# Performance work log

Hardware: AMD Instinct MI355X
Metric: run time of the kernel (lower is better)

Reference implementation:

```python
import jax, jax.numpy as jnp
import numpy as np

K = 3
HEADS = 6
EMBED = 192
KD = EMBED // HEADS  # 32
SCALE = float(KD) ** -0.5


def setup_inputs() -> dict:
    key = jax.random.key(0)
    ks = jax.random.split(key, 5)
    B, H, W, C = 8, 252, 192, 64
    x = jax.random.normal(ks[0], (B, H, W, C), dtype=jnp.float32)
    v_w = jax.random.normal(ks[1], (C, EMBED), dtype=jnp.float32) * (C ** -0.5)
    attn_w = jax.random.normal(ks[2], (C, K ** 4 * HEADS), dtype=jnp.float32) * (C ** -0.5)
    attn_b = jnp.zeros((K ** 4 * HEADS,), dtype=jnp.float32)
    out_w = jax.random.normal(ks[3], (EMBED, EMBED), dtype=jnp.float32) * (EMBED ** -0.5)
    out_b = jnp.zeros((EMBED,), dtype=jnp.float32)
    return {"x": x, "v_w": v_w, "attn_w": attn_w, "attn_b": attn_b,
            "out_w": out_w, "out_b": out_b}


def reference(x, v_w, attn_w, attn_b, out_w, out_b):
    B, H, W, C = x.shape
    hh, ww = -(-H // K), -(-W // K)          # ceil division
    ph, pw = hh * K - H, ww * K - W          # bottom/right zero padding
    xp = jnp.pad(x, ((0, 0), (0, ph), (0, pw), (0, 0))) if (ph or pw) else x

    # value branch: unfold into k*k windows -> [B, hh, ww, heads, k^2, kd]
    v = xp @ v_w
    v = v.reshape(B, hh, K, ww, K, HEADS, KD)
    v = v.transpose(0, 1, 3, 5, 2, 4, 6).reshape(B, hh, ww, HEADS, K * K, KD)

    # attention branch: k x k average pool (stride k) then dense to k^4*heads
    pooled = xp.reshape(B, hh, K, ww, K, C).mean(axis=(2, 4))  # [B, hh, ww, C]
    attn = (pooled @ attn_w + attn_b) * SCALE
    attn = attn.reshape(B, hh, ww, HEADS, K * K, K * K)
    attn = jax.nn.softmax(attn, axis=-1)

    # windowed attention: [.., k^2, k^2] @ [.., k^2, kd]
    out = attn @ v                                             # [B, hh, ww, heads, k^2, kd]

    # fold back to spatial layout, drop padding
    out = out.reshape(B, hh, ww, HEADS, K, K, KD)
    out = out.transpose(0, 1, 4, 2, 5, 3, 6).reshape(B, hh * K, ww * K, EMBED)
    out = out[:, :H, :W, :]
    return out @ out_w + out_b
```

## Files before the change

kernel.cpp:

```cpp
#include <hip/hip_runtime.h>
#include <hip/hip_bf16.h>

#define NB   8
#define NH   252
#define NW   192
#define NC   64
#define HHD  84
#define WWD  64
#define NE   192
#define NO   486
#define NWIN (NB*HHD*WWD)
#define SCALE_F 0.17677669529663687f

typedef __bf16 bf16x8 __attribute__((ext_vector_type(8)));
typedef __bf16 bf16x4 __attribute__((ext_vector_type(4)));
typedef float floatx4 __attribute__((ext_vector_type(4)));

__device__ __attribute__((aligned(16))) __hip_bfloat16 g_WT[NE * 384];
__device__ __attribute__((aligned(16))) __hip_bfloat16 g_awT[NO * 64];

__device__ __forceinline__ bf16x8 bf16x8_zero() {
    bf16x8 z;
    #pragma unroll
    for (int j = 0; j < 8; ++j) z[j] = (__bf16)0.f;
    return z;
}

__device__ __forceinline__ int koff(int t) {
    int v = 16 * t - 8;
    v = v < 0 ? 0 : v;
    return v > 48 ? 48 : v;
}

__global__ __launch_bounds__(256) void kt_prep(
    const float* __restrict__ vw, const float* __restrict__ ow,
    const float* __restrict__ aw)
{
    int t = blockIdx.x * 256 + threadIdx.x;
    if (t < NE * 384) {
        int e  = t / 384;
        int hc = t - e * 384;
        int h  = hc >> 6;
        int c  = hc & 63;
        float s = 0.f;
        #pragma unroll
        for (int d = 0; d < 32; ++d)
            s = fmaf(vw[c * NE + h * 32 + d], ow[(h * 32 + d) * NE + e], s);
        g_WT[e * 384 + hc] = __float2bfloat16(s);
    } else {
        int tt = t - NE * 384;
        if (tt < NO * 64) {
            int n = tt >> 6;
            int c = tt & 63;
            g_awT[tt] = __float2bfloat16(aw[c * NO + n]);
        }
    }
}

__global__ __launch_bounds__(256, 3) void ka_fused(
    const float* __restrict__ x,
    const float* __restrict__ attn_b,
    const float* __restrict__ out_b,
    float* __restrict__ out)
{
    __shared__ __attribute__((aligned(16))) __bf16 xwT[64 * 88];
    __shared__ __attribute__((aligned(16))) __bf16 attnA[6 * 5 * 16 * 32];
    __shared__ __attribute__((aligned(16))) __bf16 Ph[80 * 72];

    __bf16* pooledB = Ph;

    const int tid  = threadIdx.x;
    const int lane = tid & 63;
    const int wv   = tid >> 6;
    const int m16  = lane & 15;
    const int quad = lane >> 4;
    const int wbase = blockIdx.x * 8;

    const int bB   = wbase / 5376;
    const int remB = wbase - bB * 5376;
    const int iB   = remB >> 6;
    const int jB   = remB & 63;
    const int xbase = ((bB * NH + iB * 3) * NW + jB * 3) * NC;

    #pragma unroll
    for (int i = 0; i < 5; ++i) {
        int b4 = i * 4 + wv;
        bf16x4 pk;
        #pragma unroll
        for (int s = 0; s < 4; ++s) {
            int p10 = b4 * 4 + s;
            int w = p10 / 10;
            int q = p10 - w * 10;
            float xv = 0.f;
            if (q < 9) {
                int pr = q / 3;
                int pc = q - pr * 3;
                xv = x[xbase + (pr * NW + w * 3 + pc) * NC + lane];
            }
            pk[s] = (__bf16)xv;
        }
        *(bf16x4*)(&xwT[lane * 88 + b4 * 4]) = pk;
    }
    #pragma unroll
    for (int i = 0; i < 8; ++i) {
        int ch = i * 256 + tid;
        if (ch < 1920) *(uint4*)(&attnA[ch * 8]) = make_uint4(0u, 0u, 0u, 0u);
    }
    __syncthreads();

    #pragma unroll
    for (int i = 0; i < 2; ++i) {
        int win = i * 4 + wv;
        float s = 0.f;
        #pragma unroll
        for (int q = 0; q < 9; ++q) s += (float)xwT[lane * 88 + win * 10 + q];
        pooledB[win * 64 + lane] = (__bf16)(s * (1.f / 9.f));
    }
    __syncthreads();

    {
        bf16x8 afragP[2];
        #pragma unroll
        for (int ks = 0; ks < 2; ++ks)
            afragP[ks] = *(const bf16x8*)(&pooledB[m16 * 64 + ks * 32 + quad * 8]);
        const __bf16* Aw = (const __bf16*)g_awT;
        #pragma unroll
        for (int i = 0; i < 8; ++i) {
            int tile = wv * 8 + i;
            int n = tile * 16 + m16;
            bool nvalid = (tile < 31) && (n < NO);
            bf16x8 b0 = nvalid ? *(const bf16x8*)(Aw + n * 64 + quad * 8)      : bf16x8_zero();
            bf16x8 b1 = nvalid ? *(const bf16x8*)(Aw + n * 64 + 32 + quad * 8) : bf16x8_zero();
            floatx4 acc;
            acc[0] = 0.f; acc[1] = 0.f; acc[2] = 0.f; acc[3] = 0.f;
            acc = __builtin_amdgcn_mfma_f32_16x16x32_bf16(afragP[0], b0, acc, 0, 0, 0);
            acc = __builtin_amdgcn_mfma_f32_16x16x32_bf16(afragP[1], b1, acc, 0, 0, 0);
            if (nvalid && quad < 2) {
                float bn = attn_b[n];
                int h   = n / 81;
                int r81 = n - h * 81;
                int p   = r81 / 9;
                int q   = r81 - p * 9;
                #pragma unroll
                for (int r = 0; r < 4; ++r) {
                    int win = quad * 4 + r;
                    int R   = win * 10 + p;
                    int t   = R >> 4;
                    int rl  = R & 15;
                    int col = win * 10 + q - koff(t);
                    attnA[((h * 5 + t) * 16 + rl) * 32 + col] =
                        (__bf16)((acc[r] + bn) * SCALE_F);
                }
            }
        }
    }
    __syncthreads();

    #pragma unroll
    for (int it = 0; it < 2; ++it) {
        int g = it * 256 + tid;
        if (g < 432) {
            int win  = g / 54;
            int rest = g - win * 54;
            int h = rest / 9;
            int p = rest - h * 9;
            int R  = win * 10 + p;
            int t  = R >> 4;
            int rl = R & 15;
            int cb = win * 10 - koff(t);
            __bf16* a = &attnA[((h * 5 + t) * 16 + rl) * 32 + cb];
            float v[9];
            float m = -1e30f;
            #pragma unroll
            for (int q = 0; q < 9; ++q) { v[q] = (float)a[q]; m = fmaxf(m, v[q]); }
            float ssum = 0.f;
            #pragma unroll
            for (int q = 0; q < 9; ++q) { v[q] = __expf(v[q] - m); ssum += v[q]; }
            float inv = 1.f / ssum;
            #pragma unroll
            for (int q = 0; q < 9; ++q) a[q] = (__bf16)(v[q] * inv);
        }
    }
    __syncthreads();

    bf16x8 bfragX[5];
    #pragma unroll
    for (int t = 0; t < 5; ++t)
        bfragX[t] = *(const bf16x8*)(&xwT[(wv * 16 + m16) * 88 + koff(t) + quad * 8]);

    float bias[3];
    #pragma unroll
    for (int nt = 0; nt < 3; ++nt) bias[nt] = out_b[wv * 48 + nt * 16 + m16];

    floatx4 accF[5][3];
    #pragma unroll
    for (int mt = 0; mt < 5; ++mt)
        #pragma unroll
        for (int nt = 0; nt < 3; ++nt) {
            accF[mt][nt][0] = 0.f; accF[mt][nt][1] = 0.f;
            accF[mt][nt][2] = 0.f; accF[mt][nt][3] = 0.f;
        }

    const __bf16* Wt = (const __bf16*)g_WT;

    #pragma unroll
    for (int h = 0; h < 6; ++h) {
        {
            floatx4 accP[5];
            #pragma unroll
            for (int mt = 0; mt < 5; ++mt) {
                accP[mt][0] = 0.f; accP[mt][1] = 0.f;
                accP[mt][2] = 0.f; accP[mt][3] = 0.f;
                bf16x8 af = *(const bf16x8*)(&attnA[((h * 5 + mt) * 16 + m16) * 32 + quad * 8]);
                accP[mt] = __builtin_amdgcn_mfma_f32_16x16x32_bf16(af, bfragX[mt], accP[mt], 0, 0, 0);
            }
            #pragma unroll
            for (int mt = 0; mt < 5; ++mt)
                #pragma unroll
                for (int r = 0; r < 4; ++r)
                    Ph[(mt * 16 + quad * 4 + r) * 72 + wv * 16 + m16] = (__bf16)accP[mt][r];
        }
        __syncthreads();

        #pragma unroll
        for (int ks = 0; ks < 2; ++ks) {
            bf16x8 bw[3];
            #pragma unroll
            for (int nt = 0; nt < 3; ++nt)
                bw[nt] = *(const bf16x8*)(Wt + (wv * 48 + nt * 16 + m16) * 384 + h * 64 + ks * 32 + quad * 8);
            #pragma unroll
            for (int mt = 0; mt < 5; ++mt) {
                bf16x8 af = *(const bf16x8*)(&Ph[(mt * 16 + m16) * 72 + ks * 32 + quad * 8]);
                #pragma unroll
                for (int nt = 0; nt < 3; ++nt)
                    accF[mt][nt] = __builtin_amdgcn_mfma_f32_16x16x32_bf16(af, bw[nt], accF[mt][nt], 0, 0, 0);
            }
        }
        if (h < 5) __syncthreads();
    }

    const int obase = ((bB * NH + iB * 3) * NW + jB * 3) * NE;
    #pragma unroll
    for (int mt = 0; mt < 5; ++mt)
        #pragma unroll
        for (int r = 0; r < 4; ++r) {
            int row = mt * 16 + quad * 4 + r;
            int win = row / 10;
            int p   = row - win * 10;
            if (p < 9) {
                int pr = p / 3;
                int pc = p - pr * 3;
                int base = obase + (pr * NW + win * 3 + pc) * NE;
                #pragma unroll
                for (int nt = 0; nt < 3; ++nt)
                    out[base + wv * 48 + nt * 16 + m16] = accF[mt][nt][r] + bias[nt];
            }
        }
}

extern "C" void kernel_launch(void* const* d_in, const int* in_sizes, int n_in,
                              void* d_out, int out_size, void* d_ws, size_t ws_size,
                              hipStream_t stream)
{
    const float* x      = (const float*)d_in[0];
    const float* v_w    = (const float*)d_in[1];
    const float* attn_w = (const float*)d_in[2];
    const float* attn_b = (const float*)d_in[3];
    const float* out_w  = (const float*)d_in[4];
    const float* out_b  = (const float*)d_in[5];
    float* out = (float*)d_out;
    (void)d_ws; (void)ws_size; (void)in_sizes; (void)n_in; (void)out_size;

    hipLaunchKernelGGL(kt_prep, dim3(410), dim3(256), 0, stream, v_w, out_w, attn_w);
    hipLaunchKernelGGL(ka_fused, dim3(NWIN / 8), dim3(256), 0, stream,
                       x, attn_b, out_b, out);
}
```

Before: 558.6 us.

## Shrink LDS with compact attention buffer and swizzled layouts for higher occupancy

Stores the full softmax attention scores compactly, then rebuilds a single per-head block-diagonal operand before each head's MFMA step instead of keeping all six heads pre-expanded. This cuts shared-memory use so the kernel can target 4 blocks per CU instead of 3. It also XOR-swizzles the transposed x tile and pads other LDS strides to reduce bank conflicts. The attention-times-value MFMA operands are swapped so results are written as packed 4-element stores. The trade-off is an extra scatter pass per head, which adds LDS traffic and integer index math inside the head loop.

```diff
diff --git a/kernel.cpp b/kernel.cpp
--- a/kernel.cpp
+++ b/kernel.cpp
@@ -5,11 +5,9 @@
 #define NH   252
 #define NW   192
 #define NC   64
-#define HHD  84
-#define WWD  64
 #define NE   192
 #define NO   486
-#define NWIN (NB*HHD*WWD)
+#define NWIN (NB*84*64)
 #define SCALE_F 0.17677669529663687f
 
 typedef __bf16 bf16x8 __attribute__((ext_vector_type(8)));
@@ -30,6 +28,17 @@
     int v = 16 * t - 8;
     v = v < 0 ? 0 : v;
     return v > 48 ? 48 : v;
+}
+
+__device__ __forceinline__ int xw_idx(int c, int p) {
+    return c * 128 + ((((p) >> 3) ^ (c & 15)) << 3) + ((p) & 7);
+}
+
+__device__ __forceinline__ bf16x8 ld_b64x2(const __bf16* p) {
+    union { bf16x4 h[2]; bf16x8 v; } u;
+    u.h[0] = *(const bf16x4*)p;
+    u.h[1] = *(const bf16x4*)(p + 4);
+    return u.v;
 }
 
 __global__ __launch_bounds__(256) void kt_prep(
@@ -57,17 +66,18 @@
     }
 }
 
-__global__ __launch_bounds__(256, 3) void ka_fused(
+__global__ __launch_bounds__(256, 4) void ka_fused(
     const float* __restrict__ x,
     const float* __restrict__ attn_b,
     const float* __restrict__ out_b,
     float* __restrict__ out)
 {
-    __shared__ __attribute__((aligned(16))) __bf16 xwT[64 * 88];
-    __shared__ __attribute__((aligned(16))) __bf16 attnA[6 * 5 * 16 * 32];
-    __shared__ __attribute__((aligned(16))) __bf16 Ph[80 * 72];
-
-    __bf16* pooledB = Ph;
+    __shared__ __attribute__((aligned(16))) __bf16 xwT[64 * 128];
+    __shared__ __attribute__((aligned(16))) __bf16 attnS[8 * 486];
+    __shared__ __attribute__((aligned(16))) __bf16 attnBD[5 * 16 * 36];
+    __shared__ __attribute__((aligned(16))) __bf16 PhS[80 * 68];
+
+    __bf16* pooled = PhS;
 
     const int tid  = threadIdx.x;
     const int lane = tid & 63;
@@ -99,12 +109,12 @@
             }
             pk[s] = (__bf16)xv;
         }
-        *(bf16x4*)(&xwT[lane * 88 + b4 * 4]) = pk;
-    }
-    #pragma unroll
-    for (int i = 0; i < 8; ++i) {
+        *(bf16x4*)(&xwT[lane * 128 + (((b4 >> 1) ^ (lane & 15)) << 3) + (b4 & 1) * 4]) = pk;
+    }
+    #pragma unroll
+    for (int i = 0; i < 2; ++i) {
         int ch = i * 256 + tid;
-        if (ch < 1920) *(uint4*)(&attnA[ch * 8]) = make_uint4(0u, 0u, 0u, 0u);
+        if (ch < 360) *(uint4*)(&attnBD[ch * 8]) = make_uint4(0u, 0u, 0u, 0u);
     }
     __syncthreads();
 
@@ -113,8 +123,8 @@
         int win = i * 4 + wv;
         float s = 0.f;
         #pragma unroll
-        for (int q = 0; q < 9; ++q) s += (float)xwT[lane * 88 + win * 10 + q];
-        pooledB[win * 64 + lane] = (__bf16)(s * (1.f / 9.f));
+        for (int q = 0; q < 9; ++q) s += (float)xwT[xw_idx(lane, win * 10 + q)];
+        pooled[win * 72 + lane] = (__bf16)(s * (1.f / 9.f));
     }
     __syncthreads();
 
@@ -122,7 +132,7 @@
         bf16x8 afragP[2];
         #pragma unroll
         for (int ks = 0; ks < 2; ++ks)
-            afragP[ks] = *(const bf16x8*)(&pooledB[m16 * 64 + ks * 32 + quad * 8]);
+            afragP[ks] = *(const bf16x8*)(&pooled[m16 * 72 + ks * 32 + quad * 8]);
         const __bf16* Aw = (const __bf16*)g_awT;
         #pragma unroll
         for (int i = 0; i < 8; ++i) {
@@ -137,20 +147,9 @@
             acc = __builtin_amdgcn_mfma_f32_16x16x32_bf16(afragP[1], b1, acc, 0, 0, 0);
             if (nvalid && quad < 2) {
                 float bn = attn_b[n];
-                int h   = n / 81;
-                int r81 = n - h * 81;
-                int p   = r81 / 9;
-                int q   = r81 - p * 9;
                 #pragma unroll
-                for (int r = 0; r < 4; ++r) {
-                    int win = quad * 4 + r;
-                    int R   = win * 10 + p;
-                    int t   = R >> 4;
-                    int rl  = R & 15;
-                    int col = win * 10 + q - koff(t);
-                    attnA[((h * 5 + t) * 16 + rl) * 32 + col] =
-                        (__bf16)((acc[r] + bn) * SCALE_F);
-                }
+                for (int r = 0; r < 4; ++r)
+                    attnS[(quad * 4 + r) * 486 + n] = (__bf16)((acc[r] + bn) * SCALE_F);
             }
         }
     }
@@ -158,17 +157,11 @@
 
     #pragma unroll
     for (int it = 0; it < 2; ++it) {
-        int g = it * 256 + tid;
-        if (g < 432) {
-            int win  = g / 54;
-            int rest = g - win * 54;
-            int h = rest / 9;
-            int p = rest - h * 9;
-            int R  = win * 10 + p;
-            int t  = R >> 4;
-            int rl = R & 15;
-            int cb = win * 10 - koff(t);
-            __bf16* a = &attnA[((h * 5 + t) * 16 + rl) * 32 + cb];
+        int t = it * 256 + tid;
+        if (t < 432) {
+            int win = t / 54;
+            int g = t - win * 54;
+            __bf16* a = &attnS[win * 486 + g * 9];
             float v[9];
             float m = -1e30f;
             #pragma unroll
@@ -185,8 +178,11 @@
 
     bf16x8 bfragX[5];
     #pragma unroll
-    for (int t = 0; t < 5; ++t)
-        bfragX[t] = *(const bf16x8*)(&xwT[(wv * 16 + m16) * 88 + koff(t) + quad * 8]);
+    for (int nt = 0; nt < 5; ++nt) {
+        int c  = wv * 16 + m16;
+        int p0 = koff(nt) + quad * 8;
+        bfragX[nt] = *(const bf16x8*)(&xwT[c * 128 + (((p0 >> 3) ^ (c & 15)) << 3)]);
+    }
 
     float bias[3];
     #pragma unroll
@@ -201,6 +197,22 @@
             accF[mt][nt][2] = 0.f; accF[mt][nt][3] = 0.f;
         }
 
+    #pragma unroll
+    for (int it = 0; it < 3; ++it) {
+        int t = it * 256 + tid;
+        if (t < 648) {
+            int win = t / 81;
+            int r81 = t - win * 81;
+            int p = r81 / 9;
+            int q = r81 - p * 9;
+            int R  = win * 10 + p;
+            int tt = R >> 4;
+            int rl = R & 15;
+            attnBD[(tt * 16 + rl) * 36 + win * 10 + q - koff(tt)] = attnS[win * 486 + r81];
+        }
+    }
+    __syncthreads();
+
     const __bf16* Wt = (const __bf16*)g_WT;
 
     #pragma unroll
@@ -208,17 +220,19 @@
         {
             floatx4 accP[5];
             #pragma unroll
-            for (int mt = 0; mt < 5; ++mt) {
-                accP[mt][0] = 0.f; accP[mt][1] = 0.f;
-                accP[mt][2] = 0.f; accP[mt][3] = 0.f;
-                bf16x8 af = *(const bf16x8*)(&attnA[((h * 5 + mt) * 16 + m16) * 32 + quad * 8]);
-                accP[mt] = __builtin_amdgcn_mfma_f32_16x16x32_bf16(af, bfragX[mt], accP[mt], 0, 0, 0);
-            }
-            #pragma unroll
-            for (int mt = 0; mt < 5; ++mt)
+            for (int nt = 0; nt < 5; ++nt) {
+                accP[nt][0] = 0.f; accP[nt][1] = 0.f;
+                accP[nt][2] = 0.f; accP[nt][3] = 0.f;
+                bf16x8 bfrag = ld_b64x2(&attnBD[(nt * 16 + m16) * 36 + quad * 8]);
+                accP[nt] = __builtin_amdgcn_mfma_f32_16x16x32_bf16(bfragX[nt], bfrag, accP[nt], 0, 0, 0);
+            }
+            #pragma unroll
+            for (int nt = 0; nt < 5; ++nt) {
+                bf16x4 pk;
                 #pragma unroll
-                for (int r = 0; r < 4; ++r)
-                    Ph[(mt * 16 + quad * 4 + r) * 72 + wv * 16 + m16] = (__bf16)accP[mt][r];
+                for (int r = 0; r < 4; ++r) pk[r] = (__bf16)accP[nt][r];
+                *(bf16x4*)(&PhS[(nt * 16 + m16) * 68 + wv * 16 + quad * 4]) = pk;
+            }
         }
         __syncthreads();
 
@@ -230,13 +244,30 @@
                 bw[nt] = *(const bf16x8*)(Wt + (wv * 48 + nt * 16 + m16) * 384 + h * 64 + ks * 32 + quad * 8);
             #pragma unroll
             for (int mt = 0; mt < 5; ++mt) {
-                bf16x8 af = *(const bf16x8*)(&Ph[(mt * 16 + m16) * 72 + ks * 32 + quad * 8]);
+                bf16x8 af = ld_b64x2(&PhS[(mt * 16 + m16) * 68 + ks * 32 + quad * 8]);
                 #pragma unroll
                 for (int nt = 0; nt < 3; ++nt)
                     accF[mt][nt] = __builtin_amdgcn_mfma_f32_16x16x32_bf16(af, bw[nt], accF[mt][nt], 0, 0, 0);
             }
         }
-        if (h < 5) __syncthreads();
+        if (h < 5) {
+            #pragma unroll
+            for (int it = 0; it < 3; ++it) {
+                int t = it * 256 + tid;
+                if (t < 648) {
+                    int win = t / 81;
+                    int r81 = t - win * 81;
+                    int p = r81 / 9;
+                    int q = r81 - p * 9;
+                    int R  = win * 10 + p;
+                    int tt = R >> 4;
+                    int rl = R & 15;
+                    attnBD[(tt * 16 + rl) * 36 + win * 10 + q - koff(tt)] =
+                        attnS[win * 486 + (h + 1) * 81 + r81];
+                }
+            }
+            __syncthreads();
+        }
     }
 
     const int obase = ((bB * NH + iB * 3) * NW + jB * 3) * NE;
```

Result: no change. 551.3 us (-1.3%).
